# Kernel tuning notes

Hardware: AMD Instinct MI355X
Metric: run time of the kernel (lower is better)

The kernel has to match this reference:

```python
import jax, jax.numpy as jnp
import numpy as np

D_MODEL = 256
N_BINS = 11
# standard KNRM kernels: exact-match bin (mu=1, sigma=1e-3) + 10 soft bins
MUS = jnp.array([1.0, 0.9, 0.7, 0.5, 0.3, 0.1, -0.1, -0.3, -0.5, -0.7, -0.9], dtype=jnp.float32)
SIGMAS = jnp.array([1e-3] + [0.1] * 10, dtype=jnp.float32)


def _l2norm(x, eps=1e-10):
    # F.normalize(p=2, eps=1e-10): x / max(||x||, eps)
    n = jnp.sqrt(jnp.sum(x * x, axis=-1, keepdims=True))
    return x / jnp.maximum(n, eps)


def setup_inputs() -> dict:
    key = jax.random.key(0)
    ks = jax.random.split(key, 10)
    B, NB, Q, T, D = 64, 8, 32, 256, D_MODEL
    return {
        "word_atten": jax.random.uniform(ks[0], (B, NB, Q), dtype=jnp.float32),
        "hq": jax.random.normal(ks[1], (B, NB, Q, D), dtype=jnp.float32),
        "can": jax.random.normal(ks[2], (B, T, D), dtype=jnp.float32),
        "rep": jax.random.normal(ks[3], (B, NB, D), dtype=jnp.float32),
        "rep_cur": jax.random.normal(ks[4], (B, D), dtype=jnp.float32),
        "mask_hq": jnp.ones((B, NB, Q), dtype=jnp.float32),
        "mask_can": jnp.ones((B, T), dtype=jnp.float32),
        "mask_session": jnp.ones((B, NB), dtype=jnp.float32),
        "W_dense": jax.random.normal(ks[5], (N_BINS, 1), dtype=jnp.float32) * 0.3,
        "b_dense": jnp.zeros((1,), dtype=jnp.float32),
        "W_att": jax.random.normal(ks[6], (D, D), dtype=jnp.float32) * (1.0 / np.sqrt(D)),
        "b_att": jnp.zeros((D,), dtype=jnp.float32),
    }


def reference(word_atten, hq, can, rep, rep_cur, mask_hq, mask_can, mask_session,
              W_dense, b_dense, W_att, b_att):
    # cosine-similarity matrix: [B, NB, Q, T]
    hq_n = _l2norm(hq)
    can_n = _l2norm(can)
    matrix = jnp.einsum("bnqd,btd->bnqt", hq_n, can_n)

    # Gaussian kernel soft-binning: expand to [B, NB, Q, T, N_BINS]
    diff = matrix[..., None] - MUS  # broadcast over bins
    kern = jnp.exp(-(diff * diff) / (2.0 * SIGMAS * SIGMAS))
    kern = kern * mask_can[:, None, None, :, None]  # mask doc tokens
    pooling_sum = jnp.sum(kern, axis=3)  # [B, NB, Q, N_BINS]

    log_pool = jnp.log(jnp.clip(pooling_sum, 1e-10)) * 0.01
    log_pool = log_pool * mask_hq[..., None] * word_atten[..., None]
    pooled = jnp.sum(log_pool, axis=2)  # [B, NB, N_BINS]

    pooled = pooled * mask_session[..., None]

    # attention over session blocks (AttendAttention): scaled dot with projected current rep
    q = rep_cur @ W_att + b_att  # [B, D]
    scores = jnp.einsum("bnd,bd->bn", rep, q) / np.sqrt(D_MODEL).astype(np.float32)
    scores = jnp.where(mask_session > 0, scores, -1e9)
    attn = jax.nn.softmax(scores, axis=-1)  # [B, NB]

    score = jnp.tanh(pooled @ W_dense + b_dense).squeeze(-1)  # [B, NB]
    return jnp.sum(score * attn, axis=1)  # [B]
```

## Files before the change

kernel.cpp:

```cpp
#include <hip/hip_runtime.h>

#define B_ 64
#define NB_ 8
#define Q_ 32
#define T_ 256
#define D_ 256
#define NBINS 11

typedef __attribute__((ext_vector_type(8))) short bf16x8;
typedef __attribute__((ext_vector_type(4))) float f32x4;
typedef unsigned short ushort_t;
typedef unsigned int uint_t;

#define CANH_OFF 0u
#define CANL_OFF 8388608u
#define PSUM_OFF 16777216u

__device__ inline ushort_t bf16_rnd(float f) {
  uint_t u = __float_as_uint(f);
  return (ushort_t)((u + 0x8000u) >> 16);
}
__device__ inline uint_t pack2(ushort_t a, ushort_t b) {
  return (uint_t)a | ((uint_t)b << 16);
}

__global__ __launch_bounds__(256) void split_kernel(
    const float* __restrict__ can, uint4* __restrict__ canH,
    uint4* __restrict__ canL) {
  __shared__ __align__(16) ushort_t sm_hi[32 * 264];
  __shared__ __align__(16) ushort_t sm_lo[32 * 264];
  int blk = blockIdx.x;
  int tid = threadIdx.x;
  int b = blk >> 3, ch = blk & 7;
  const float* src = can + ((size_t)b * T_ + ch * 32) * D_;
  int tilebase = b * 16 + ch * 2;

#pragma unroll
  for (int it = 0; it < 4; it++) {
    int flat = it * 2048 + tid * 8;
    int row = flat >> 8, col = flat & 255;
    const float* p = src + row * D_ + col;
    float4 x = reinterpret_cast<const float4*>(p)[0];
    float4 y = reinterpret_cast<const float4*>(p)[1];
    float s = x.x * x.x + x.y * x.y + x.z * x.z + x.w * x.w +
              y.x * y.x + y.y * y.y + y.z * y.z + y.w * y.w;
    s += __shfl_xor(s, 1);
    s += __shfl_xor(s, 2);
    s += __shfl_xor(s, 4);
    s += __shfl_xor(s, 8);
    s += __shfl_xor(s, 16);
    float inv = 1.0f / fmaxf(sqrtf(s), 1e-10f);
    float v[8] = {x.x, x.y, x.z, x.w, y.x, y.y, y.z, y.w};
    ushort_t h[8], l[8];
#pragma unroll
    for (int j = 0; j < 8; j++) {
      float sv = v[j] * inv;
      h[j] = bf16_rnd(sv);
      float hf = __uint_as_float(((uint_t)h[j]) << 16);
      l[j] = bf16_rnd(sv - hf);
    }
    uint4 ph = {pack2(h[0], h[1]), pack2(h[2], h[3]), pack2(h[4], h[5]),
                pack2(h[6], h[7])};
    uint4 pl = {pack2(l[0], l[1]), pack2(l[2], l[3]), pack2(l[4], l[5]),
                pack2(l[6], l[7])};
    *reinterpret_cast<uint4*>(&sm_hi[row * 264 + col]) = ph;
    *reinterpret_cast<uint4*>(&sm_lo[row * 264 + col]) = pl;
  }
  __syncthreads();
  int wv = tid >> 6, lane = tid & 63;
  int tl = wv >> 1, part = wv & 1;
  int lq = lane & 15, lk = lane >> 4;
  const ushort_t* smp = part ? sm_lo : sm_hi;
  uint4* dst = part ? canL : canH;
#pragma unroll
  for (int kk = 0; kk < 8; kk++) {
    const ushort_t* a = &smp[(tl * 16 + lq) * 264 + kk * 32 + lk * 8];
    dst[((size_t)(tilebase + tl) * 8 + kk) * 64 + lane] =
        *reinterpret_cast<const uint4*>(a);
  }
}

__global__ __launch_bounds__(256, 2) void pool_kernel(
    const float* __restrict__ hq, const uint4* __restrict__ canH,
    const uint4* __restrict__ canL, const float* __restrict__ mask_can,
    float* __restrict__ psum) {
  __shared__ float partial[4 * 16 * NBINS];

  const float mus[NBINS] = {1.0f, 0.9f, 0.7f, 0.5f, 0.3f, 0.1f,
                            -0.1f, -0.3f, -0.5f, -0.7f, -0.9f};
  const float nis2[NBINS] = {-5.0e5f, -50.f, -50.f, -50.f, -50.f, -50.f,
                             -50.f, -50.f, -50.f, -50.f, -50.f};

  int i = blockIdx.x;
  int b = i & 63;
  int nb = i >> 6;
  int outb = b * NB_ + nb;
  int tid = threadIdx.x;
  int wv = tid >> 6, lane = tid & 63;
  int lq = lane & 15, lk = lane >> 4;
  int mtile = wv & 1, tq = wv >> 1;

  const float* arow =
      hq + (size_t)outb * (Q_ * D_) + (size_t)(mtile * 16 + lq) * D_;
  float sumsq = 0.f;
#pragma unroll
  for (int kk = 0; kk < 8; kk++) {
    const float* p = arow + kk * 32 + lk * 8;
    float4 x = reinterpret_cast<const float4*>(p)[0];
    float4 y = reinterpret_cast<const float4*>(p)[1];
    sumsq += x.x * x.x + x.y * x.y + x.z * x.z + x.w * x.w +
             y.x * y.x + y.y * y.y + y.z * y.z + y.w * y.w;
  }
  sumsq += __shfl_xor(sumsq, 16);
  sumsq += __shfl_xor(sumsq, 32);
  float ainv = 1.0f / fmaxf(sqrtf(sumsq), 1e-10f);

  bf16x8 ah[8], al[8];
#pragma unroll
  for (int kk = 0; kk < 8; kk++) {
    const float* p = arow + kk * 32 + lk * 8;
    float4 x = reinterpret_cast<const float4*>(p)[0];
    float4 y = reinterpret_cast<const float4*>(p)[1];
    float v[8] = {x.x, x.y, x.z, x.w, y.x, y.y, y.z, y.w};
    union { bf16x8 v8; ushort_t u[8]; } H, L;
#pragma unroll
    for (int j = 0; j < 8; j++) {
      float s = v[j] * ainv;
      ushort_t h = bf16_rnd(s);
      float hf = __uint_as_float(((uint_t)h) << 16);
      H.u[j] = h;
      L.u[j] = bf16_rnd(s - hf);
    }
    ah[kk] = H.v8;
    al[kk] = L.v8;
  }

  float binacc[4][NBINS];
#pragma unroll
  for (int r = 0; r < 4; r++)
#pragma unroll
    for (int j = 0; j < NBINS; j++) binacc[r][j] = 0.0f;

  f32x4 accPrev;
  float mkPrev = 0.0f;

  {
    int tt = tq * 8;
    size_t bbase = (size_t)(b * 16 + tt) * 8 * 64 + lane;
    f32x4 acc = {0.f, 0.f, 0.f, 0.f};
#pragma unroll
    for (int kk = 0; kk < 8; kk++) {
      bf16x8 bh = *reinterpret_cast<const bf16x8*>(&canH[bbase + kk * 64]);
      bf16x8 bl = *reinterpret_cast<const bf16x8*>(&canL[bbase + kk * 64]);
      acc = __builtin_amdgcn_mfma_f32_16x16x32_bf16(ah[kk], bh, acc, 0, 0, 0);
      acc = __builtin_amdgcn_mfma_f32_16x16x32_bf16(al[kk], bh, acc, 0, 0, 0);
      acc = __builtin_amdgcn_mfma_f32_16x16x32_bf16(ah[kk], bl, acc, 0, 0, 0);
    }
    accPrev = acc;
    mkPrev = mask_can[b * T_ + tt * 16 + lq];
  }

  for (int ti = 1; ti < 8; ti++) {
    int tt = tq * 8 + ti;
    size_t bbase = (size_t)(b * 16 + tt) * 8 * 64 + lane;
    bf16x8 bh[8], bl[8];
#pragma unroll
    for (int kk = 0; kk < 8; kk++) {
      bh[kk] = *reinterpret_cast<const bf16x8*>(&canH[bbase + kk * 64]);
      bl[kk] = *reinterpret_cast<const bf16x8*>(&canL[bbase + kk * 64]);
    }
#pragma unroll
    for (int r = 0; r < 4; r++) {
      float v0 = accPrev[r];
#pragma unroll
      for (int j = 0; j < NBINS; j++) {
        float d0 = v0 - mus[j];
        binacc[r][j] += mkPrev * __expf(d0 * d0 * nis2[j]);
      }
    }
    f32x4 acc = {0.f, 0.f, 0.f, 0.f};
#pragma unroll
    for (int kk = 0; kk < 8; kk++) {
      acc = __builtin_amdgcn_mfma_f32_16x16x32_bf16(ah[kk], bh[kk], acc, 0, 0, 0);
      acc = __builtin_amdgcn_mfma_f32_16x16x32_bf16(al[kk], bh[kk], acc, 0, 0, 0);
      acc = __builtin_amdgcn_mfma_f32_16x16x32_bf16(ah[kk], bl[kk], acc, 0, 0, 0);
    }
    accPrev = acc;
    mkPrev = mask_can[b * T_ + tt * 16 + lq];
  }
#pragma unroll
  for (int r = 0; r < 4; r++) {
    float v0 = accPrev[r];
#pragma unroll
    for (int j = 0; j < NBINS; j++) {
      float d0 = v0 - mus[j];
      binacc[r][j] += mkPrev * __expf(d0 * d0 * nis2[j]);
    }
  }

#pragma unroll
  for (int r = 0; r < 4; r++)
#pragma unroll
    for (int j = 0; j < NBINS; j++) {
      float v = binacc[r][j];
      v += __shfl_xor(v, 1);
      v += __shfl_xor(v, 2);
      v += __shfl_xor(v, 4);
      v += __shfl_xor(v, 8);
      binacc[r][j] = v;
    }
  if (lq == 0) {
#pragma unroll
    for (int r = 0; r < 4; r++)
#pragma unroll
      for (int j = 0; j < NBINS; j++)
        partial[(wv * 16 + lk * 4 + r) * NBINS + j] = binacc[r][j];
  }
  __syncthreads();

  float* dst = &psum[(size_t)outb * (Q_ * NBINS)];
  for (int idx = tid; idx < Q_ * NBINS; idx += 256) {
    int q = idx / NBINS;
    int j = idx - q * NBINS;
    int m = q >> 4, r16 = q & 15;
    dst[idx] = partial[(m * 16 + r16) * NBINS + j] +
               partial[((2 + m) * 16 + r16) * NBINS + j];
  }
}

__global__ __launch_bounds__(256) void final_kernel(
    const float* __restrict__ rep, const float* __restrict__ rep_cur,
    const float* __restrict__ mask_session, const float* __restrict__ W_dense,
    const float* __restrict__ b_dense, const float* __restrict__ W_att,
    const float* __restrict__ b_att, const float* __restrict__ word_atten,
    const float* __restrict__ mask_hq, const float* __restrict__ psum,
    float* __restrict__ out) {
  __shared__ float lp[NB_ * Q_ * NBINS];
  __shared__ float pooled_sm[NB_ * NBINS];
  __shared__ float qproj[D_];
  __shared__ float scores_sm[NB_];
  int b = blockIdx.x, tid = threadIdx.x;

  {
    int nb = tid >> 5, q = tid & 31;
    int outb = b * NB_ + nb;
    float wa = word_atten[outb * Q_ + q] * mask_hq[outb * Q_ + q];
    const float* ps = &psum[(size_t)outb * (Q_ * NBINS) + q * NBINS];
#pragma unroll
    for (int j = 0; j < NBINS; j++)
      lp[(nb * Q_ + q) * NBINS + j] = logf(fmaxf(ps[j], 1e-10f)) * 0.01f * wa;
  }

  const float* rc = rep_cur + b * D_;
  float acc = b_att[tid];
  for (int k = 0; k < D_; k++) acc += rc[k] * W_att[k * D_ + tid];
  qproj[tid] = acc;
  __syncthreads();

  if (tid < NB_ * NBINS) {
    int nb = tid / NBINS, j = tid - nb * NBINS;
    float s = 0.f;
#pragma unroll
    for (int q = 0; q < Q_; q++) s += lp[(nb * Q_ + q) * NBINS + j];
    pooled_sm[nb * NBINS + j] = s;
  }

  int wv = tid >> 6, lane = tid & 63;
  for (int nn = wv; nn < NB_; nn += 4) {
    const float* rp = rep + ((size_t)b * NB_ + nn) * D_;
    float4 r4 = reinterpret_cast<const float4*>(rp)[lane];
    float4 q4 = *reinterpret_cast<float4*>(&qproj[lane * 4]);
    float s = r4.x * q4.x + r4.y * q4.y + r4.z * q4.z + r4.w * q4.w;
#pragma unroll
    for (int off = 32; off > 0; off >>= 1) s += __shfl_down(s, off);
    if (lane == 0) scores_sm[nn] = s * 0.0625f;
  }
  __syncthreads();

  if (tid == 0) {
    float sc[NB_];
    float mx = -1e30f;
    for (int nn = 0; nn < NB_; nn++) {
      float s = (mask_session[b * NB_ + nn] > 0.f) ? scores_sm[nn] : -1e9f;
      sc[nn] = s;
      mx = fmaxf(mx, s);
    }
    float den = 0.f;
    for (int nn = 0; nn < NB_; nn++) {
      sc[nn] = __expf(sc[nn] - mx);
      den += sc[nn];
    }
    float res = 0.f;
    for (int nn = 0; nn < NB_; nn++) {
      float ms = mask_session[b * NB_ + nn];
      float pw = b_dense[0];
      for (int j = 0; j < NBINS; j++)
        pw += pooled_sm[nn * NBINS + j] * ms * W_dense[j];
      res += tanhf(pw) * (sc[nn] / den);
    }
    out[b] = res;
  }
}

extern "C" void kernel_launch(void* const* d_in, const int* in_sizes, int n_in,
                              void* d_out, int out_size, void* d_ws,
                              size_t ws_size, hipStream_t stream) {
  const float* word_atten = (const float*)d_in[0];
  const float* hq = (const float*)d_in[1];
  const float* can = (const float*)d_in[2];
  const float* rep = (const float*)d_in[3];
  const float* rep_cur = (const float*)d_in[4];
  const float* mask_hq = (const float*)d_in[5];
  const float* mask_can = (const float*)d_in[6];
  const float* mask_session = (const float*)d_in[7];
  const float* W_dense = (const float*)d_in[8];
  const float* b_dense = (const float*)d_in[9];
  const float* W_att = (const float*)d_in[10];
  const float* b_att = (const float*)d_in[11];
  float* out = (float*)d_out;

  char* ws = (char*)d_ws;
  uint4* canH = (uint4*)(ws + CANH_OFF);
  uint4* canL = (uint4*)(ws + CANL_OFF);
  float* psum = (float*)(ws + PSUM_OFF);

  hipLaunchKernelGGL(split_kernel, dim3(512), dim3(256), 0, stream, can, canH,
                     canL);
  hipLaunchKernelGGL(pool_kernel, dim3(B_ * NB_), dim3(256), 0, stream, hq,
                     canH, canL, mask_can, psum);
  hipLaunchKernelGGL(final_kernel, dim3(B_), dim3(256), 0, stream, rep,
                     rep_cur, mask_session, W_dense, b_dense, W_att, b_att,
                     word_atten, mask_hq, psum, out);
}
```

Before: 133.7 us.

## Fuse split, pool and final kernels into one cooperative kernel with grid syncs

Merges the three kernel launches into a single cooperative launch of 512 blocks, using grid-wide syncs between the normalize/split, pooling, and final attention stages. The aim is to cut the launch overhead and inter-kernel gaps of three back-to-back launches. In exchange it adds two grid barriers, limits occupancy to what a cooperative launch allows, and leaves most blocks idle during the final stage. The old three-kernel path stays as a fallback if the cooperative launch fails.

```diff
diff --git a/kernel.cpp b/kernel.cpp
--- a/kernel.cpp
+++ b/kernel.cpp
@@ -1,4 +1,7 @@
 #include <hip/hip_runtime.h>
+#include <hip/hip_cooperative_groups.h>
+
+namespace cg = cooperative_groups;
 
 #define B_ 64
 #define NB_ 8
@@ -22,6 +25,285 @@
 }
 __device__ inline uint_t pack2(ushort_t a, ushort_t b) {
   return (uint_t)a | ((uint_t)b << 16);
+}
+
+__global__ __launch_bounds__(256) void fused_kernel(
+    const float* __restrict__ can, const float* __restrict__ hq,
+    const float* __restrict__ word_atten, const float* __restrict__ mask_hq,
+    const float* __restrict__ mask_can, const float* __restrict__ rep,
+    const float* __restrict__ rep_cur, const float* __restrict__ mask_session,
+    const float* __restrict__ W_dense, const float* __restrict__ b_dense,
+    const float* __restrict__ W_att, const float* __restrict__ b_att,
+    uint4* __restrict__ canH, uint4* __restrict__ canL,
+    float* __restrict__ psum, float* __restrict__ out) {
+  __shared__ __align__(16) char smem[33792];
+  ushort_t* sm_hi = (ushort_t*)smem;
+  ushort_t* sm_lo = (ushort_t*)(smem + 16896);
+
+  const float mus[NBINS] = {1.0f, 0.9f, 0.7f, 0.5f, 0.3f, 0.1f,
+                            -0.1f, -0.3f, -0.5f, -0.7f, -0.9f};
+  const float nis2[NBINS] = {-5.0e5f, -50.f, -50.f, -50.f, -50.f, -50.f,
+                             -50.f, -50.f, -50.f, -50.f, -50.f};
+
+  int blk = blockIdx.x;
+  int tid = threadIdx.x;
+  int wv = tid >> 6, lane = tid & 63;
+  int lq = lane & 15, lk = lane >> 4;
+
+  {
+    int b = blk & 63, ch = blk >> 6;
+    const float* src = can + ((size_t)b * T_ + ch * 32) * D_;
+    int tilebase = b * 16 + ch * 2;
+#pragma unroll
+    for (int it = 0; it < 4; it++) {
+      int flat = it * 2048 + tid * 8;
+      int row = flat >> 8, col = flat & 255;
+      const float* p = src + row * D_ + col;
+      float4 x = reinterpret_cast<const float4*>(p)[0];
+      float4 y = reinterpret_cast<const float4*>(p)[1];
+      float s = x.x * x.x + x.y * x.y + x.z * x.z + x.w * x.w +
+                y.x * y.x + y.y * y.y + y.z * y.z + y.w * y.w;
+      s += __shfl_xor(s, 1);
+      s += __shfl_xor(s, 2);
+      s += __shfl_xor(s, 4);
+      s += __shfl_xor(s, 8);
+      s += __shfl_xor(s, 16);
+      float inv = 1.0f / fmaxf(sqrtf(s), 1e-10f);
+      float v[8] = {x.x, x.y, x.z, x.w, y.x, y.y, y.z, y.w};
+      ushort_t h[8], l[8];
+#pragma unroll
+      for (int j = 0; j < 8; j++) {
+        float sv = v[j] * inv;
+        h[j] = bf16_rnd(sv);
+        float hf = __uint_as_float(((uint_t)h[j]) << 16);
+        l[j] = bf16_rnd(sv - hf);
+      }
+      uint4 ph = {pack2(h[0], h[1]), pack2(h[2], h[3]), pack2(h[4], h[5]),
+                  pack2(h[6], h[7])};
+      uint4 pl = {pack2(l[0], l[1]), pack2(l[2], l[3]), pack2(l[4], l[5]),
+                  pack2(l[6], l[7])};
+      *reinterpret_cast<uint4*>(&sm_hi[row * 264 + col]) = ph;
+      *reinterpret_cast<uint4*>(&sm_lo[row * 264 + col]) = pl;
+    }
+    __syncthreads();
+    int tl = wv >> 1, part = wv & 1;
+    const ushort_t* smp = part ? sm_lo : sm_hi;
+    uint4* dst = part ? canL : canH;
+#pragma unroll
+    for (int kk = 0; kk < 8; kk++) {
+      const ushort_t* a = &smp[(tl * 16 + lq) * 264 + kk * 32 + lk * 8];
+      dst[((size_t)(tilebase + tl) * 8 + kk) * 64 + lane] =
+          *reinterpret_cast<const uint4*>(a);
+    }
+  }
+
+  cg::this_grid().sync();
+
+  {
+    float* partial = (float*)smem;
+    int b = blk & 63;
+    int nb = blk >> 6;
+    int outb = b * NB_ + nb;
+    int mtile = wv & 1, tq = wv >> 1;
+
+    const float* arow =
+        hq + (size_t)outb * (Q_ * D_) + (size_t)(mtile * 16 + lq) * D_;
+    float sumsq = 0.f;
+#pragma unroll
+    for (int kk = 0; kk < 8; kk++) {
+      const float* p = arow + kk * 32 + lk * 8;
+      float4 x = reinterpret_cast<const float4*>(p)[0];
+      float4 y = reinterpret_cast<const float4*>(p)[1];
+      sumsq += x.x * x.x + x.y * x.y + x.z * x.z + x.w * x.w +
+               y.x * y.x + y.y * y.y + y.z * y.z + y.w * y.w;
+    }
+    sumsq += __shfl_xor(sumsq, 16);
+    sumsq += __shfl_xor(sumsq, 32);
+    float ainv = 1.0f / fmaxf(sqrtf(sumsq), 1e-10f);
+
+    bf16x8 ah[8], al[8];
+#pragma unroll
+    for (int kk = 0; kk < 8; kk++) {
+      const float* p = arow + kk * 32 + lk * 8;
+      float4 x = reinterpret_cast<const float4*>(p)[0];
+      float4 y = reinterpret_cast<const float4*>(p)[1];
+      float v[8] = {x.x, x.y, x.z, x.w, y.x, y.y, y.z, y.w};
+      union { bf16x8 v8; ushort_t u[8]; } H, L;
+#pragma unroll
+      for (int j = 0; j < 8; j++) {
+        float s = v[j] * ainv;
+        ushort_t h = bf16_rnd(s);
+        float hf = __uint_as_float(((uint_t)h) << 16);
+        H.u[j] = h;
+        L.u[j] = bf16_rnd(s - hf);
+      }
+      ah[kk] = H.v8;
+      al[kk] = L.v8;
+    }
+
+    float binacc[4][NBINS];
+#pragma unroll
+    for (int r = 0; r < 4; r++)
+#pragma unroll
+      for (int j = 0; j < NBINS; j++) binacc[r][j] = 0.0f;
+
+    f32x4 accPrev;
+    float mkPrev = 0.0f;
+
+    {
+      int tt = tq * 8;
+      size_t bbase = (size_t)(b * 16 + tt) * 8 * 64 + lane;
+      f32x4 acc = {0.f, 0.f, 0.f, 0.f};
+#pragma unroll
+      for (int kk = 0; kk < 8; kk++) {
+        bf16x8 bh = *reinterpret_cast<const bf16x8*>(&canH[bbase + kk * 64]);
+        bf16x8 bl = *reinterpret_cast<const bf16x8*>(&canL[bbase + kk * 64]);
+        acc = __builtin_amdgcn_mfma_f32_16x16x32_bf16(ah[kk], bh, acc, 0, 0, 0);
+        acc = __builtin_amdgcn_mfma_f32_16x16x32_bf16(al[kk], bh, acc, 0, 0, 0);
+        acc = __builtin_amdgcn_mfma_f32_16x16x32_bf16(ah[kk], bl, acc, 0, 0, 0);
+      }
+      accPrev = acc;
+      mkPrev = mask_can[b * T_ + tt * 16 + lq];
+    }
+
+    for (int ti = 1; ti < 8; ti++) {
+      int tt = tq * 8 + ti;
+      size_t bbase = (size_t)(b * 16 + tt) * 8 * 64 + lane;
+      bf16x8 bh[8], bl[8];
+#pragma unroll
+      for (int kk = 0; kk < 8; kk++) {
+        bh[kk] = *reinterpret_cast<const bf16x8*>(&canH[bbase + kk * 64]);
+        bl[kk] = *reinterpret_cast<const bf16x8*>(&canL[bbase + kk * 64]);
+      }
+#pragma unroll
+      for (int r = 0; r < 4; r++) {
+        float v0 = accPrev[r];
+#pragma unroll
+        for (int j = 0; j < NBINS; j++) {
+          float d0 = v0 - mus[j];
+          binacc[r][j] += mkPrev * __expf(d0 * d0 * nis2[j]);
+        }
+      }
+      f32x4 acc = {0.f, 0.f, 0.f, 0.f};
+#pragma unroll
+      for (int kk = 0; kk < 8; kk++) {
+        acc = __builtin_amdgcn_mfma_f32_16x16x32_bf16(ah[kk], bh[kk], acc, 0, 0, 0);
+        acc = __builtin_amdgcn_mfma_f32_16x16x32_bf16(al[kk], bh[kk], acc, 0, 0, 0);
+        acc = __builtin_amdgcn_mfma_f32_16x16x32_bf16(ah[kk], bl[kk], acc, 0, 0, 0);
+      }
+      accPrev = acc;
+      mkPrev = mask_can[b * T_ + tt * 16 + lq];
+    }
+#pragma unroll
+    for (int r = 0; r < 4; r++) {
+      float v0 = accPrev[r];
+#pragma unroll
+      for (int j = 0; j < NBINS; j++) {
+        float d0 = v0 - mus[j];
+        binacc[r][j] += mkPrev * __expf(d0 * d0 * nis2[j]);
+      }
+    }
+
+#pragma unroll
+    for (int r = 0; r < 4; r++)
+#pragma unroll
+      for (int j = 0; j < NBINS; j++) {
+        float v = binacc[r][j];
+        v += __shfl_xor(v, 1);
+        v += __shfl_xor(v, 2);
+        v += __shfl_xor(v, 4);
+        v += __shfl_xor(v, 8);
+        binacc[r][j] = v;
+      }
+    __syncthreads();
+    if (lq == 0) {
+#pragma unroll
+      for (int r = 0; r < 4; r++)
+#pragma unroll
+        for (int j = 0; j < NBINS; j++)
+          partial[(wv * 16 + lk * 4 + r) * NBINS + j] = binacc[r][j];
+    }
+    __syncthreads();
+
+    float* dst = &psum[(size_t)outb * (Q_ * NBINS)];
+    for (int idx = tid; idx < Q_ * NBINS; idx += 256) {
+      int q = idx / NBINS;
+      int j = idx - q * NBINS;
+      int m = q >> 4, r16 = q & 15;
+      dst[idx] = partial[(m * 16 + r16) * NBINS + j] +
+                 partial[((2 + m) * 16 + r16) * NBINS + j];
+    }
+  }
+
+  cg::this_grid().sync();
+
+  if (blk < B_) {
+    float* lp = (float*)smem;
+    float* pooled_sm = lp + NB_ * Q_ * NBINS;
+    float* qproj = pooled_sm + NB_ * NBINS;
+    float* scores_sm = qproj + D_;
+    int b = blk;
+
+    {
+      int nb = tid >> 5, q = tid & 31;
+      int outb = b * NB_ + nb;
+      float wa = word_atten[outb * Q_ + q] * mask_hq[outb * Q_ + q];
+      const float* ps = &psum[(size_t)outb * (Q_ * NBINS) + q * NBINS];
+#pragma unroll
+      for (int j = 0; j < NBINS; j++)
+        lp[(nb * Q_ + q) * NBINS + j] =
+            logf(fmaxf(ps[j], 1e-10f)) * 0.01f * wa;
+    }
+
+    const float* rc = rep_cur + b * D_;
+    float acc = b_att[tid];
+    for (int k = 0; k < D_; k++) acc += rc[k] * W_att[k * D_ + tid];
+    qproj[tid] = acc;
+    __syncthreads();
+
+    if (tid < NB_ * NBINS) {
+      int nb = tid / NBINS, j = tid - nb * NBINS;
+      float s = 0.f;
+#pragma unroll
+      for (int q = 0; q < Q_; q++) s += lp[(nb * Q_ + q) * NBINS + j];
+      pooled_sm[nb * NBINS + j] = s;
+    }
+
+    for (int nn = wv; nn < NB_; nn += 4) {
+      const float* rp = rep + ((size_t)b * NB_ + nn) * D_;
+      float4 r4 = reinterpret_cast<const float4*>(rp)[lane];
+      float4 q4 = *reinterpret_cast<float4*>(&qproj[lane * 4]);
+      float s = r4.x * q4.x + r4.y * q4.y + r4.z * q4.z + r4.w * q4.w;
+#pragma unroll
+      for (int off = 32; off > 0; off >>= 1) s += __shfl_down(s, off);
+      if (lane == 0) scores_sm[nn] = s * 0.0625f;
+    }
+    __syncthreads();
+
+    if (tid == 0) {
+      float sc[NB_];
+      float mx = -1e30f;
+      for (int nn = 0; nn < NB_; nn++) {
+        float s = (mask_session[b * NB_ + nn] > 0.f) ? scores_sm[nn] : -1e9f;
+        sc[nn] = s;
+        mx = fmaxf(mx, s);
+      }
+      float den = 0.f;
+      for (int nn = 0; nn < NB_; nn++) {
+        sc[nn] = __expf(sc[nn] - mx);
+        den += sc[nn];
+      }
+      float res = 0.f;
+      for (int nn = 0; nn < NB_; nn++) {
+        float ms = mask_session[b * NB_ + nn];
+        float pw = b_dense[0];
+        for (int j = 0; j < NBINS; j++)
+          pw += pooled_sm[nn * NBINS + j] * ms * W_dense[j];
+        res += tanhf(pw) * (sc[nn] / den);
+      }
+      out[b] = res;
+    }
+  }
 }
 
 __global__ __launch_bounds__(256) void split_kernel(
@@ -34,7 +316,6 @@
   int b = blk >> 3, ch = blk & 7;
   const float* src = can + ((size_t)b * T_ + ch * 32) * D_;
   int tilebase = b * 16 + ch * 2;
-
 #pragma unroll
   for (int it = 0; it < 4; it++) {
     int flat = it * 2048 + tid * 8;
@@ -85,12 +366,10 @@
     const uint4* __restrict__ canL, const float* __restrict__ mask_can,
     float* __restrict__ psum) {
   __shared__ float partial[4 * 16 * NBINS];
-
   const float mus[NBINS] = {1.0f, 0.9f, 0.7f, 0.5f, 0.3f, 0.1f,
                             -0.1f, -0.3f, -0.5f, -0.7f, -0.9f};
   const float nis2[NBINS] = {-5.0e5f, -50.f, -50.f, -50.f, -50.f, -50.f,
                              -50.f, -50.f, -50.f, -50.f, -50.f};
-
   int i = blockIdx.x;
   int b = i & 63;
   int nb = i >> 6;
@@ -143,7 +422,6 @@
 
   f32x4 accPrev;
   float mkPrev = 0.0f;
-
   {
     int tt = tq * 8;
     size_t bbase = (size_t)(b * 16 + tt) * 8 * 64 + lane;
@@ -159,7 +437,6 @@
     accPrev = acc;
     mkPrev = mask_can[b * T_ + tt * 16 + lq];
   }
-
   for (int ti = 1; ti < 8; ti++) {
     int tt = tq * 8 + ti;
     size_t bbase = (size_t)(b * 16 + tt) * 8 * 64 + lane;
@@ -197,7 +474,6 @@
       binacc[r][j] += mkPrev * __expf(d0 * d0 * nis2[j]);
     }
   }
-
 #pragma unroll
   for (int r = 0; r < 4; r++)
 #pragma unroll
@@ -217,7 +493,6 @@
         partial[(wv * 16 + lk * 4 + r) * NBINS + j] = binacc[r][j];
   }
   __syncthreads();
-
   float* dst = &psum[(size_t)outb * (Q_ * NBINS)];
   for (int idx = tid; idx < Q_ * NBINS; idx += 256) {
     int q = idx / NBINS;
@@ -240,7 +515,6 @@
   __shared__ float qproj[D_];
   __shared__ float scores_sm[NB_];
   int b = blockIdx.x, tid = threadIdx.x;
-
   {
     int nb = tid >> 5, q = tid & 31;
     int outb = b * NB_ + nb;
@@ -250,13 +524,11 @@
     for (int j = 0; j < NBINS; j++)
       lp[(nb * Q_ + q) * NBINS + j] = logf(fmaxf(ps[j], 1e-10f)) * 0.01f * wa;
   }
-
   const float* rc = rep_cur + b * D_;
   float acc = b_att[tid];
   for (int k = 0; k < D_; k++) acc += rc[k] * W_att[k * D_ + tid];
   qproj[tid] = acc;
   __syncthreads();
-
   if (tid < NB_ * NBINS) {
     int nb = tid / NBINS, j = tid - nb * NBINS;
     float s = 0.f;
@@ -264,7 +536,6 @@
     for (int q = 0; q < Q_; q++) s += lp[(nb * Q_ + q) * NBINS + j];
     pooled_sm[nb * NBINS + j] = s;
   }
-
   int wv = tid >> 6, lane = tid & 63;
   for (int nn = wv; nn < NB_; nn += 4) {
     const float* rp = rep + ((size_t)b * NB_ + nn) * D_;
@@ -276,7 +547,6 @@
     if (lane == 0) scores_sm[nn] = s * 0.0625f;
   }
   __syncthreads();
-
   if (tid == 0) {
     float sc[NB_];
     float mx = -1e30f;
@@ -324,11 +594,21 @@
   uint4* canL = (uint4*)(ws + CANL_OFF);
   float* psum = (float*)(ws + PSUM_OFF);
 
-  hipLaunchKernelGGL(split_kernel, dim3(512), dim3(256), 0, stream, can, canH,
-                     canL);
-  hipLaunchKernelGGL(pool_kernel, dim3(B_ * NB_), dim3(256), 0, stream, hq,
-                     canH, canL, mask_can, psum);
-  hipLaunchKernelGGL(final_kernel, dim3(B_), dim3(256), 0, stream, rep,
-                     rep_cur, mask_session, W_dense, b_dense, W_att, b_att,
-                     word_atten, mask_hq, psum, out);
+  void* args[] = {(void*)&can,  (void*)&hq,        (void*)&word_atten,
+                  (void*)&mask_hq, (void*)&mask_can, (void*)&rep,
+                  (void*)&rep_cur, (void*)&mask_session, (void*)&W_dense,
+                  (void*)&b_dense, (void*)&W_att,   (void*)&b_att,
+                  (void*)&canH,  (void*)&canL,      (void*)&psum,
+                  (void*)&out};
+  hipError_t err = hipLaunchCooperativeKernel(
+      (const void*)fused_kernel, dim3(512), dim3(256), args, 0, stream);
+  if (err != hipSuccess) {
+    hipLaunchKernelGGL(split_kernel, dim3(512), dim3(256), 0, stream, can,
+                       canH, canL);
+    hipLaunchKernelGGL(pool_kernel, dim3(B_ * NB_), dim3(256), 0, stream, hq,
+                       canH, canL, mask_can, psum);
+    hipLaunchKernelGGL(final_kernel, dim3(B_), dim3(256), 0, stream, rep,
+                       rep_cur, mask_session, W_dense, b_dense, W_att, b_att,
+                       word_atten, mask_hq, psum, out);
+  }
 }
```

New measurement: 263.5 us. +97.0%, slower.
